# Kernel tuning notes

Hardware: AMD Instinct MI355X
Metric: run time of the kernel (lower is better)

Reference implementation:

```python
import jax, jax.numpy as jnp
import numpy as np

N_GRAPHS = 256
RATIO = 0.5


def setup_inputs() -> dict:
    key = jax.random.key(0)
    k0, k1, k2, k3, k4 = jax.random.split(key, 5)
    N, E, D = 100000, 1600000, 64
    x = jax.random.normal(k0, (N, D), dtype=jnp.float32)
    edge_index = jax.random.randint(k1, (2, E), 0, N, dtype=jnp.int32)
    batch = jnp.sort(jax.random.randint(k2, (N,), 0, N_GRAPHS, dtype=jnp.int32))
    # GraphConv(in_channels=64, out_channels=1) parameters
    w_rel = jax.random.normal(k3, (D,), dtype=jnp.float32) * 0.1
    b_rel = jnp.zeros((), dtype=jnp.float32)
    w_root = jax.random.normal(k4, (D,), dtype=jnp.float32) * 0.1
    return {"x": x, "edge_index": edge_index, "batch": batch,
            "w_rel": w_rel, "b_rel": b_rel, "w_root": w_root}


def reference(x, edge_index, batch, w_rel, b_rel, w_root):
    N = x.shape[0]
    src, dst = edge_index[0], edge_index[1]
    # GraphConv score: lin_rel(sum_{j in N(i)} x_j) + lin_root(x_i)
    agg = jax.ops.segment_sum(x[src], dst, num_segments=N)        # [N, D]
    score = jnp.tanh(agg @ w_rel + b_rel + x @ w_root)            # [N], SAGPool tanh
    # per-graph topk: keep k_g = ceil(ratio * n_g) highest-score nodes
    sizes = jax.ops.segment_sum(jnp.ones(N, jnp.int32), batch,
                                num_segments=N_GRAPHS)            # [G]
    k = jnp.ceil(RATIO * sizes.astype(jnp.float32)).astype(jnp.int32)
    starts = jnp.concatenate([jnp.zeros(1, jnp.int32),
                              jnp.cumsum(sizes)[:-1].astype(jnp.int32)])
    order = jnp.lexsort((-score, batch))                          # graph-major, score desc
    rank = jnp.arange(N, dtype=jnp.int32) - starts[batch[order]]  # rank within graph
    keep_sorted = rank < k[batch[order]]
    keep = jnp.zeros(N, dtype=bool).at[order].set(keep_sorted)
    # kept nodes are scaled by their tanh score; dropped nodes contribute 0
    w = jnp.where(keep, score, jnp.zeros_like(score))             # [N]
    num = jax.ops.segment_sum(x * w[:, None], batch, num_segments=N_GRAPHS)
    cnt = jax.ops.segment_sum(keep.astype(x.dtype), batch, num_segments=N_GRAPHS)
    return num / jnp.maximum(cnt, 1.0)[:, None]                   # global_mean_pool
```

## Files before the change

### kernel.cpp

```cpp
#include <hip/hip_runtime.h>

#define NGRAPHS 256
#define CHUNK 2048
#define BINR 256
#define CAPB 6144
#define MAXB 512
#define NMAX 2048

__global__ __launch_bounds__(256) void k1_fused(
    const float* __restrict__ x,
    const int*   __restrict__ batch,
    const int*   __restrict__ ei,
    const float* __restrict__ w_rel,
    const float* __restrict__ w_root,
    float* __restrict__ p, float* __restrict__ r,
    int* __restrict__ starts, int* __restrict__ ends,
    int* __restrict__ C,
    int N, int E, int NBLKE, int NBINS, int vecE)
{
    __shared__ int hist[MAXB];
    int tid = threadIdx.x;

    if ((int)blockIdx.x < NBLKE) {
        for (int b = tid; b < NBINS; b += 256) hist[b] = 0;
        __syncthreads();
        int beg = blockIdx.x * CHUNK;
        int end = min(beg + CHUNK, E);
        if (vecE) {
            const int4* d4 = (const int4*)(ei + E);
            for (int i = (beg >> 2) + tid; i < (end >> 2); i += 256) {
                int4 d = d4[i];
                atomicAdd(&hist[d.x >> 8], 1);
                atomicAdd(&hist[d.y >> 8], 1);
                atomicAdd(&hist[d.z >> 8], 1);
                atomicAdd(&hist[d.w >> 8], 1);
            }
        } else {
            for (int i = beg + tid; i < end; i += 256)
                atomicAdd(&hist[ei[E + i] >> 8], 1);
        }
        __syncthreads();
        for (int b = tid; b < NBINS; b += 256)
            C[(size_t)blockIdx.x * NBINS + b] = hist[b];
        return;
    }

    int row = ((int)blockIdx.x - NBLKE) * 16 + (tid >> 4);
    int fq  = tid & 15;
    if (row >= N) return;
    if (fq == 0) {
        int b = batch[row];
        if (row == 0) {
            for (int g = 0; g < b; ++g) { starts[g] = 0; ends[g] = 0; }
            starts[b] = 0;
        } else {
            int bp = batch[row - 1];
            if (bp != b) {
                ends[bp] = row;
                for (int g = bp + 1; g < b; ++g) { starts[g] = row; ends[g] = row; }
                starts[b] = row;
            }
        }
        if (row == N - 1) {
            ends[b] = N;
            for (int g = b + 1; g < NGRAPHS; ++g) { starts[g] = N; ends[g] = N; }
        }
    }
    float4 v  = *(const float4*)(x + (size_t)row * 64 + fq * 4);
    float4 wr = ((const float4*)w_rel)[fq];
    float4 wo = ((const float4*)w_root)[fq];
    float a = v.x * wr.x + v.y * wr.y + v.z * wr.z + v.w * wr.w;
    float c = v.x * wo.x + v.y * wo.y + v.z * wo.z + v.w * wo.w;
    a += __shfl_down(a, 8); c += __shfl_down(c, 8);
    a += __shfl_down(a, 4); c += __shfl_down(c, 4);
    a += __shfl_down(a, 2); c += __shfl_down(c, 2);
    a += __shfl_down(a, 1); c += __shfl_down(c, 1);
    if (fq == 0) { p[row] = a; r[row] = c; }
}

__global__ __launch_bounds__(1024) void kA2_scan(
    int* __restrict__ C, int* __restrict__ cursor, int NBLK, int NBINS)
{
    __shared__ int sh[1024];
    int b = blockIdx.x;
    int t = threadIdx.x;
    int c = (t < NBLK) ? C[(size_t)t * NBINS + b] : 0;
    sh[t] = c;
    __syncthreads();
    #pragma unroll
    for (int off = 1; off < 1024; off <<= 1) {
        int v = (t >= off) ? sh[t - off] : 0;
        __syncthreads();
        sh[t] += v;
        __syncthreads();
    }
    if (t < NBLK) C[(size_t)t * NBINS + b] = b * CAPB + (sh[t] - c);
    if (t == 1023) cursor[b] = sh[t];
}

__global__ __launch_bounds__(256) void kA3_scatter(
    const int* __restrict__ ei,
    const int* __restrict__ C,
    unsigned* __restrict__ bucket,
    int E, int NBINS, int vecE)
{
    __shared__ int cur[MAXB];
    int tid = threadIdx.x;
    for (int b = tid; b < NBINS; b += 256)
        cur[b] = C[(size_t)blockIdx.x * NBINS + b];
    __syncthreads();
    int beg = blockIdx.x * CHUNK;
    int end = min(beg + CHUNK, E);
    if (vecE) {
        const int4* s4 = (const int4*)ei;
        const int4* d4 = (const int4*)(ei + E);
        for (int i = (beg >> 2) + tid; i < (end >> 2); i += 256) {
            int4 d = d4[i];
            int4 s = s4[i];
            int b0 = d.x >> 8, p0 = atomicAdd(&cur[b0], 1);
            if (p0 < (b0 + 1) * CAPB) bucket[p0] = ((unsigned)s.x << 8) | (unsigned)(d.x & 255);
            int b1 = d.y >> 8, p1 = atomicAdd(&cur[b1], 1);
            if (p1 < (b1 + 1) * CAPB) bucket[p1] = ((unsigned)s.y << 8) | (unsigned)(d.y & 255);
            int b2 = d.z >> 8, p2 = atomicAdd(&cur[b2], 1);
            if (p2 < (b2 + 1) * CAPB) bucket[p2] = ((unsigned)s.z << 8) | (unsigned)(d.z & 255);
            int b3 = d.w >> 8, p3 = atomicAdd(&cur[b3], 1);
            if (p3 < (b3 + 1) * CAPB) bucket[p3] = ((unsigned)s.w << 8) | (unsigned)(d.w & 255);
        }
    } else {
        for (int i = beg + tid; i < end; i += 256) {
            int d = ei[E + i];
            int s = ei[i];
            int b = d >> 8;
            int pos = atomicAdd(&cur[b], 1);
            if (pos < (b + 1) * CAPB)
                bucket[pos] = ((unsigned)s << 8) | (unsigned)(d & 255);
        }
    }
}

__global__ __launch_bounds__(512) void kB_score(
    const unsigned* __restrict__ bucket,
    const int* __restrict__ cursor,
    const float* __restrict__ p,
    const float* __restrict__ r,
    const float* __restrict__ brel,
    float* __restrict__ score, int N)
{
    __shared__ float acc[BINR];
    int tid = threadIdx.x;
    int b   = blockIdx.x;
    if (tid < BINR) acc[tid] = 0.0f;
    __syncthreads();
    int lo  = b * CAPB;
    int cnt = min(cursor[b], CAPB);
    const uint2* bk2 = (const uint2*)(bucket + lo);
    int half = cnt >> 1;
    for (int e = tid; e < half; e += 512) {
        uint2 u = bk2[e];
        atomicAdd(&acc[u.x & 255u], p[u.x >> 8]);
        atomicAdd(&acc[u.y & 255u], p[u.y >> 8]);
    }
    if (tid == 0 && (cnt & 1)) {
        unsigned u = bucket[lo + cnt - 1];
        atomicAdd(&acc[u & 255u], p[u >> 8]);
    }
    __syncthreads();
    int node = b * BINR + tid;
    if (tid < BINR && node < N)
        score[node] = tanhf(acc[tid] + brel[0] + r[node]);
}

__global__ __launch_bounds__(256) void kZ_zero(float* __restrict__ a, int N)
{
    int i = blockIdx.x * 256 + threadIdx.x;
    if (i < N) a[i] = 0.0f;
}
__global__ __launch_bounds__(256) void k2_scatter(
    const int* __restrict__ ei, const float* __restrict__ p,
    float* aggdot, int E)
{
    int i = blockIdx.x * 256 + threadIdx.x;
    if (i < E) unsafeAtomicAdd(&aggdot[ei[E + i]], p[ei[i]]);
}
__global__ __launch_bounds__(256) void kS_score(
    const float* __restrict__ aggdot, const float* __restrict__ r,
    const float* __restrict__ brel, float* __restrict__ score, int N)
{
    int i = blockIdx.x * 256 + threadIdx.x;
    if (i < N) score[i] = tanhf(aggdot[i] + brel[0] + r[i]);
}

__global__ __launch_bounds__(512) void k4_pool(
    const float* __restrict__ x,
    const float* __restrict__ score,
    const int* __restrict__ starts,
    const int* __restrict__ ends,
    float* __restrict__ out)
{
    __shared__ float sc[NMAX];
    __shared__ int   kidx[NMAX / 2 + 64];
    __shared__ float kw[NMAX / 2 + 64];
    __shared__ float accs[8][64][4];
    __shared__ int   pctr;

    int g   = blockIdx.x;
    int tid = threadIdx.x;
    int start = starts[g];
    int n     = ends[g] - start;
    if (n > NMAX) n = NMAX;
    int k = (n + 1) >> 1;
    if (tid == 0) pctr = 0;

    for (int i = tid; i < n; i += 512) sc[i] = score[start + i];
    __syncthreads();

    for (int i = tid; i < n; i += 512) {
        float si = sc[i];
        int rank = 0;
        for (int j = 0; j < n; ++j) {
            float sj = sc[j];
            rank += (sj > si) || (sj == si && j < i);
        }
        if (rank < k) {
            int pos = atomicAdd(&pctr, 1);
            kidx[pos] = i;
            kw[pos]   = si;
        }
    }
    __syncthreads();
    int k32 = (k + 31) & ~31;
    for (int e = k + tid; e < k32; e += 512) { kidx[e] = 0; kw[e] = 0.0f; }
    __syncthreads();

    int wg   = tid >> 6;
    int lane = tid & 63;
    int rgrp = lane >> 4;
    int fq   = lane & 15;
    float a0 = 0.0f, a1 = 0.0f, a2 = 0.0f, a3 = 0.0f;
    #pragma unroll 2
    for (int e = wg * 4 + rgrp; e < k32; e += 32) {
        float wv = kw[e];
        int row  = start + kidx[e];
        const float4 v = *(const float4*)(x + (size_t)row * 64 + fq * 4);
        a0 += v.x * wv; a1 += v.y * wv; a2 += v.z * wv; a3 += v.w * wv;
    }
    accs[wg][lane][0] = a0; accs[wg][lane][1] = a1;
    accs[wg][lane][2] = a2; accs[wg][lane][3] = a3;
    __syncthreads();
    if (tid < 64) {
        int f = tid;
        float sum = 0.0f;
        #pragma unroll
        for (int gg = 0; gg < 8; ++gg)
            #pragma unroll
            for (int rg = 0; rg < 4; ++rg)
                sum += accs[gg][rg * 16 + (f >> 2)][f & 3];
        out[(size_t)g * 64 + f] = sum / fmaxf((float)k, 1.0f);
    }
}

extern "C" void kernel_launch(void* const* d_in, const int* in_sizes, int n_in,
                              void* d_out, int out_size, void* d_ws, size_t ws_size,
                              hipStream_t stream) {
    const float* x      = (const float*)d_in[0];
    const int*   ei     = (const int*)  d_in[1];
    const int*   batch  = (const int*)  d_in[2];
    const float* w_rel  = (const float*)d_in[3];
    const float* b_rel  = (const float*)d_in[4];
    const float* w_root = (const float*)d_in[5];
    float* out = (float*)d_out;

    int N = in_sizes[2];
    int E = in_sizes[1] / 2;
    int NBLKE = (E + CHUNK - 1) / CHUNK;
    int NBINS = (N + BINR - 1) / BINR;
    int vecE  = ((E & 3) == 0);

    float* p      = (float*)d_ws;
    float* r      = p + (size_t)N;
    float* score  = r + (size_t)N;
    int*   starts = (int*)(score + (size_t)N);
    int*   ends   = starts + NGRAPHS;
    int*   cursor = ends + NGRAPHS;
    int*   C      = cursor + MAXB;
    unsigned* bucket = (unsigned*)(C + (size_t)NBLKE * NBINS);
    size_t need = ((size_t)3 * N + 2 * NGRAPHS + MAXB
                   + (size_t)NBLKE * NBINS + (size_t)NBINS * CAPB) * 4;

    bool binned = (need <= ws_size) && (NBLKE <= 1024) && (NBINS <= MAXB)
                  && (N < (1 << 24));

    int dotblks = (N + 15) / 16;
    if (binned) {
        k1_fused<<<NBLKE + dotblks, 256, 0, stream>>>(x, batch, ei, w_rel, w_root,
                                                      p, r, starts, ends, C,
                                                      N, E, NBLKE, NBINS, vecE);
        kA2_scan<<<NBINS, 1024, 0, stream>>>(C, cursor, NBLKE, NBINS);
        kA3_scatter<<<NBLKE, 256, 0, stream>>>(ei, C, bucket, E, NBINS, vecE);
        kB_score<<<NBINS, 512, 0, stream>>>(bucket, cursor, p, r, b_rel, score, N);
    } else {
        float* aggdot = (float*)C;
        k1_fused<<<dotblks, 256, 0, stream>>>(x, batch, ei, w_rel, w_root,
                                              p, r, starts, ends, C, N, E, 0,
                                              NBINS, vecE);
        kZ_zero<<<(N + 255) / 256, 256, 0, stream>>>(aggdot, N);
        k2_scatter<<<(E + 255) / 256, 256, 0, stream>>>(ei, p, aggdot, E);
        kS_score<<<(N + 255) / 256, 256, 0, stream>>>(aggdot, r, b_rel, score, N);
    }
    k4_pool<<<NGRAPHS, 512, 0, stream>>>(x, score, starts, ends, out);
}
```

Baseline: 139.2 us.

## Replace global histogram scan with per-block atomic bin reservation

Binning the edges previously took three passes: a per-block histogram, a column scan over the block×bin count matrix, and a scatter. Now each block computes its local histogram and reserves space in each bin with one global atomicAdd on a cursor that the dot kernel initialises to b*CAPB. This drops the scan kernel, the count matrix and one kernel launch, at the cost of reading the edge list twice within a block and nondeterministic order inside each bin. Separately, the top-k rank loop in the pool kernel now reads shared memory as float4 and handles four candidates per iteration.

```diff
diff --git a/kernel.cpp b/kernel.cpp
--- a/kernel.cpp
+++ b/kernel.cpp
@@ -7,45 +7,22 @@
 #define MAXB 512
 #define NMAX 2048
 
-__global__ __launch_bounds__(256) void k1_fused(
+__global__ __launch_bounds__(256) void k1_dots(
     const float* __restrict__ x,
     const int*   __restrict__ batch,
-    const int*   __restrict__ ei,
     const float* __restrict__ w_rel,
     const float* __restrict__ w_root,
     float* __restrict__ p, float* __restrict__ r,
     int* __restrict__ starts, int* __restrict__ ends,
-    int* __restrict__ C,
-    int N, int E, int NBLKE, int NBINS, int vecE)
-{
-    __shared__ int hist[MAXB];
-    int tid = threadIdx.x;
-
-    if ((int)blockIdx.x < NBLKE) {
-        for (int b = tid; b < NBINS; b += 256) hist[b] = 0;
-        __syncthreads();
-        int beg = blockIdx.x * CHUNK;
-        int end = min(beg + CHUNK, E);
-        if (vecE) {
-            const int4* d4 = (const int4*)(ei + E);
-            for (int i = (beg >> 2) + tid; i < (end >> 2); i += 256) {
-                int4 d = d4[i];
-                atomicAdd(&hist[d.x >> 8], 1);
-                atomicAdd(&hist[d.y >> 8], 1);
-                atomicAdd(&hist[d.z >> 8], 1);
-                atomicAdd(&hist[d.w >> 8], 1);
-            }
-        } else {
-            for (int i = beg + tid; i < end; i += 256)
-                atomicAdd(&hist[ei[E + i] >> 8], 1);
-        }
-        __syncthreads();
-        for (int b = tid; b < NBINS; b += 256)
-            C[(size_t)blockIdx.x * NBINS + b] = hist[b];
-        return;
-    }
-
-    int row = ((int)blockIdx.x - NBLKE) * 16 + (tid >> 4);
+    int* __restrict__ cursor,
+    int N, int NBINS)
+{
+    int tid = threadIdx.x;
+    if ((int)blockIdx.x < 2) {
+        int b = blockIdx.x * 256 + tid;
+        if (b < NBINS) cursor[b] = b * CAPB;
+    }
+    int row = (int)blockIdx.x * 16 + (tid >> 4);
     int fq  = tid & 15;
     if (row >= N) return;
     if (fq == 0) {
@@ -78,52 +55,52 @@
     if (fq == 0) { p[row] = a; r[row] = c; }
 }
 
-__global__ __launch_bounds__(1024) void kA2_scan(
-    int* __restrict__ C, int* __restrict__ cursor, int NBLK, int NBINS)
-{
-    __shared__ int sh[1024];
-    int b = blockIdx.x;
-    int t = threadIdx.x;
-    int c = (t < NBLK) ? C[(size_t)t * NBINS + b] : 0;
-    sh[t] = c;
-    __syncthreads();
-    #pragma unroll
-    for (int off = 1; off < 1024; off <<= 1) {
-        int v = (t >= off) ? sh[t - off] : 0;
-        __syncthreads();
-        sh[t] += v;
-        __syncthreads();
-    }
-    if (t < NBLK) C[(size_t)t * NBINS + b] = b * CAPB + (sh[t] - c);
-    if (t == 1023) cursor[b] = sh[t];
-}
-
-__global__ __launch_bounds__(256) void kA3_scatter(
+__global__ __launch_bounds__(256) void kA_bin(
     const int* __restrict__ ei,
-    const int* __restrict__ C,
+    int* cursor,
     unsigned* __restrict__ bucket,
     int E, int NBINS, int vecE)
 {
-    __shared__ int cur[MAXB];
-    int tid = threadIdx.x;
-    for (int b = tid; b < NBINS; b += 256)
-        cur[b] = C[(size_t)blockIdx.x * NBINS + b];
+    __shared__ int hist[MAXB];
+    __shared__ int base[MAXB];
+    int tid = threadIdx.x;
+    for (int b = tid; b < NBINS; b += 256) hist[b] = 0;
     __syncthreads();
     int beg = blockIdx.x * CHUNK;
     int end = min(beg + CHUNK, E);
+    if (vecE) {
+        const int4* d4 = (const int4*)(ei + E);
+        for (int i = (beg >> 2) + tid; i < (end >> 2); i += 256) {
+            int4 d = d4[i];
+            atomicAdd(&hist[d.x >> 8], 1);
+            atomicAdd(&hist[d.y >> 8], 1);
+            atomicAdd(&hist[d.z >> 8], 1);
+            atomicAdd(&hist[d.w >> 8], 1);
+        }
+    } else {
+        for (int i = beg + tid; i < end; i += 256)
+            atomicAdd(&hist[ei[E + i] >> 8], 1);
+    }
+    __syncthreads();
+    for (int b = tid; b < NBINS; b += 256) {
+        int c = hist[b];
+        base[b] = c ? atomicAdd(&cursor[b], c) : 0;
+        hist[b] = 0;
+    }
+    __syncthreads();
     if (vecE) {
         const int4* s4 = (const int4*)ei;
         const int4* d4 = (const int4*)(ei + E);
         for (int i = (beg >> 2) + tid; i < (end >> 2); i += 256) {
             int4 d = d4[i];
             int4 s = s4[i];
-            int b0 = d.x >> 8, p0 = atomicAdd(&cur[b0], 1);
+            int b0 = d.x >> 8, p0 = base[b0] + atomicAdd(&hist[b0], 1);
             if (p0 < (b0 + 1) * CAPB) bucket[p0] = ((unsigned)s.x << 8) | (unsigned)(d.x & 255);
-            int b1 = d.y >> 8, p1 = atomicAdd(&cur[b1], 1);
+            int b1 = d.y >> 8, p1 = base[b1] + atomicAdd(&hist[b1], 1);
             if (p1 < (b1 + 1) * CAPB) bucket[p1] = ((unsigned)s.y << 8) | (unsigned)(d.y & 255);
-            int b2 = d.z >> 8, p2 = atomicAdd(&cur[b2], 1);
+            int b2 = d.z >> 8, p2 = base[b2] + atomicAdd(&hist[b2], 1);
             if (p2 < (b2 + 1) * CAPB) bucket[p2] = ((unsigned)s.z << 8) | (unsigned)(d.z & 255);
-            int b3 = d.w >> 8, p3 = atomicAdd(&cur[b3], 1);
+            int b3 = d.w >> 8, p3 = base[b3] + atomicAdd(&hist[b3], 1);
             if (p3 < (b3 + 1) * CAPB) bucket[p3] = ((unsigned)s.w << 8) | (unsigned)(d.w & 255);
         }
     } else {
@@ -131,7 +108,7 @@
             int d = ei[E + i];
             int s = ei[i];
             int b = d >> 8;
-            int pos = atomicAdd(&cur[b], 1);
+            int pos = base[b] + atomicAdd(&hist[b], 1);
             if (pos < (b + 1) * CAPB)
                 bucket[pos] = ((unsigned)s << 8) | (unsigned)(d & 255);
         }
@@ -152,7 +129,7 @@
     if (tid < BINR) acc[tid] = 0.0f;
     __syncthreads();
     int lo  = b * CAPB;
-    int cnt = min(cursor[b], CAPB);
+    int cnt = min(cursor[b] - lo, CAPB);
     const uint2* bk2 = (const uint2*)(bucket + lo);
     int half = cnt >> 1;
     for (int e = tid; e < half; e += 512) {
@@ -214,10 +191,19 @@
     for (int i = tid; i < n; i += 512) sc[i] = score[start + i];
     __syncthreads();
 
+    int n4 = n & ~3;
     for (int i = tid; i < n; i += 512) {
         float si = sc[i];
         int rank = 0;
-        for (int j = 0; j < n; ++j) {
+        int j = 0;
+        for (; j < n4; j += 4) {
+            float4 s4 = *(const float4*)&sc[j];
+            rank += (s4.x > si) || (s4.x == si && (j + 0) < i);
+            rank += (s4.y > si) || (s4.y == si && (j + 1) < i);
+            rank += (s4.z > si) || (s4.z == si && (j + 2) < i);
+            rank += (s4.w > si) || (s4.w == si && (j + 3) < i);
+        }
+        for (; j < n; ++j) {
             float sj = sc[j];
             rank += (sj > si) || (sj == si && j < i);
         }
@@ -282,27 +268,19 @@
     int*   starts = (int*)(score + (size_t)N);
     int*   ends   = starts + NGRAPHS;
     int*   cursor = ends + NGRAPHS;
-    int*   C      = cursor + MAXB;
-    unsigned* bucket = (unsigned*)(C + (size_t)NBLKE * NBINS);
-    size_t need = ((size_t)3 * N + 2 * NGRAPHS + MAXB
-                   + (size_t)NBLKE * NBINS + (size_t)NBINS * CAPB) * 4;
-
-    bool binned = (need <= ws_size) && (NBLKE <= 1024) && (NBINS <= MAXB)
-                  && (N < (1 << 24));
+    unsigned* bucket = (unsigned*)(cursor + MAXB);
+    size_t need = ((size_t)3 * N + 2 * NGRAPHS + MAXB + (size_t)NBINS * CAPB) * 4;
+
+    bool binned = (need <= ws_size) && (NBINS <= MAXB) && (N < (1 << 24));
 
     int dotblks = (N + 15) / 16;
+    k1_dots<<<dotblks, 256, 0, stream>>>(x, batch, w_rel, w_root, p, r,
+                                         starts, ends, cursor, N, NBINS);
     if (binned) {
-        k1_fused<<<NBLKE + dotblks, 256, 0, stream>>>(x, batch, ei, w_rel, w_root,
-                                                      p, r, starts, ends, C,
-                                                      N, E, NBLKE, NBINS, vecE);
-        kA2_scan<<<NBINS, 1024, 0, stream>>>(C, cursor, NBLKE, NBINS);
-        kA3_scatter<<<NBLKE, 256, 0, stream>>>(ei, C, bucket, E, NBINS, vecE);
+        kA_bin<<<NBLKE, 256, 0, stream>>>(ei, cursor, bucket, E, NBINS, vecE);
         kB_score<<<NBINS, 512, 0, stream>>>(bucket, cursor, p, r, b_rel, score, N);
     } else {
-        float* aggdot = (float*)C;
-        k1_fused<<<dotblks, 256, 0, stream>>>(x, batch, ei, w_rel, w_root,
-                                              p, r, starts, ends, C, N, E, 0,
-                                              NBINS, vecE);
+        float* aggdot = (float*)bucket;
         kZ_zero<<<(N + 255) / 256, 256, 0, stream>>>(aggdot, N);
         k2_scatter<<<(E + 255) / 256, 256, 0, stream>>>(ei, p, aggdot, E);
         kS_score<<<(N + 255) / 256, 256, 0, stream>>>(aggdot, r, b_rel, score, N);
```

After: 144.8 us. 4.0% more time.
